# Performance work log

Hardware: AMD Instinct MI355X
Metric: run time of the kernel (lower is better)

Reference implementation:

```python
import jax, jax.numpy as jnp
import numpy as np

B, N, D, H = 4, 2048, 768, 12
DK = D // H  # 64

def setup_inputs() -> dict:
    key = jax.random.key(0)
    ks = jax.random.split(key, 7)
    f = lambda k, shape: jax.random.normal(k, shape, dtype=jnp.float32)
    return {
        "Q": f(ks[0], (B, N, D)),
        "K": f(ks[1], (B, N, D)),
        "V": f(ks[2], (B, N, D)),
        "w_q": f(ks[3], (D, D)) * 0.02,
        "w_k": f(ks[4], (D, D)) * 0.02,
        "w_v": f(ks[5], (D, D)) * 0.02,
        "w_o": f(ks[6], (D, D)) * 0.02,
    }

def reference(Q, K, V, w_q, w_k, w_v, w_o):
    # Linear with bias=False: y = x @ W.T, W is [out, in]
    def proj(x, w):
        # [B, N, D] -> [B, H, N, DK]
        y = jnp.einsum('bnd,ed->bne', x, w)
        return y.reshape(B, N, H, DK).transpose(0, 2, 1, 3)
    q = proj(Q, w_q)
    k = proj(K, w_k)
    v = proj(V, w_v)
    scale = 1.0 / jnp.sqrt(jnp.float32(DK))
    scores = jnp.einsum('bhqd,bhkd->bhqk', q, k) * scale  # [B,H,N,N]
    weights = jax.nn.softmax(scores, axis=-1)
    out = jnp.einsum('bhqk,bhkd->bhqd', weights, v)  # [B,H,N,DK]
    out = out.transpose(0, 2, 1, 3).reshape(B, N, D)
    return jnp.einsum('bnd,ed->bne', out, w_o)
```

## Files before the change

### kernel.cpp

```cpp
#include <hip/hip_runtime.h>

typedef unsigned short ushortT;
typedef __attribute__((ext_vector_type(8))) short bf16x8;
typedef __attribute__((ext_vector_type(4))) float f32x4;
typedef __attribute__((ext_vector_type(16))) float f32x16;
typedef __attribute__((ext_vector_type(2))) int i32x2;

#define QSCALE 0.18033688011112042f

__device__ __forceinline__ unsigned short f2bf(float f) {
  unsigned int u = __float_as_uint(f);
  u += 0x7FFFu + ((u >> 16) & 1u);
  return (unsigned short)(u >> 16);
}
__device__ __forceinline__ unsigned short f2bf_fast(float f) {
  unsigned int u = __float_as_uint(f) + 0x8000u;
  return (unsigned short)(u >> 16);
}

__device__ __forceinline__ void gl16(const void* g, void* l) {
  __builtin_amdgcn_global_load_lds(
      (const __attribute__((address_space(1))) void*)g,
      (__attribute__((address_space(3))) void*)l, 16, 0, 0);
}

__device__ __forceinline__ float cross_sum(float x) {
  i32x2 r = __builtin_amdgcn_permlane32_swap(__float_as_int(x), __float_as_int(x), false, false);
  return __int_as_float(r[0]) + __int_as_float(r[1]);
}
__device__ __forceinline__ unsigned cvtpk(float lo, float hi) {
  unsigned r;
  asm("v_cvt_pk_bf16_f32 %0, %1, %2" : "=v"(r) : "v"(lo), "v"(hi));
  return r;
}

__global__ __launch_bounds__(256) void cvt_all(
    const float* __restrict__ q, const float* __restrict__ k, const float* __restrict__ v,
    const float* __restrict__ w0, const float* __restrict__ w1,
    const float* __restrict__ w2, const float* __restrict__ w3,
    ushortT* xq, ushortT* xk, ushortT* xv,
    ushortT* bw0, ushortT* bw1, ushortT* bw2, ushortT* bw3) {
  int t = blockIdx.y;
  const float* src; ushortT* dst; int n;
  switch (t) {
    case 0: src = q;  dst = xq;  n = 8192 * 768; break;
    case 1: src = k;  dst = xk;  n = 8192 * 768; break;
    case 2: src = v;  dst = xv;  n = 8192 * 768; break;
    case 3: src = w0; dst = bw0; n = 768 * 768;  break;
    case 4: src = w1; dst = bw1; n = 768 * 768;  break;
    case 5: src = w2; dst = bw2; n = 768 * 768;  break;
    default: src = w3; dst = bw3; n = 768 * 768; break;
  }
  int i = (blockIdx.x * 256 + threadIdx.x) * 4;
  if (i >= n) return;
  float4 f = *(const float4*)(src + i);
  ushort4 o = make_ushort4(f2bf(f.x), f2bf(f.y), f2bf(f.z), f2bf(f.w));
  *(ushort4*)(dst + i) = o;
}

__global__ __launch_bounds__(256) void gemm_qkv(
    const ushortT* __restrict__ xq, const ushortT* __restrict__ xk,
    const ushortT* __restrict__ xv, const ushortT* __restrict__ bwq,
    const ushortT* __restrict__ bwk, const ushortT* __restrict__ bwv,
    ushortT* qp, ushortT* kp, ushortT* vtp) {
  constexpr int K = 768;
  __shared__ __attribute__((aligned(16))) ushortT As[128 * 32];
  __shared__ __attribute__((aligned(16))) ushortT Bs[128 * 32];
  const int tid = threadIdx.x;
  const int w = tid >> 6, l = tid & 63;
  const int z = blockIdx.z, bx = blockIdx.x;
  const ushortT* A;
  const ushortT* Bm;
  int m0, n0;
  if (z < 2) {
    A = z ? xk : xq; Bm = z ? bwk : bwq;
    m0 = (bx / 6) * 128; n0 = (bx % 6) * 128;
  } else {
    A = bwv; Bm = xv;
    m0 = (bx % 6) * 128; n0 = (bx / 6) * 128;
  }
  const ushortT* Ab = A  + (size_t)m0 * K;
  const ushortT* Bb = Bm + (size_t)n0 * K;

  f32x4 acc[4][4] = {};
  const int wr = w >> 1, wc = w & 1;
  const int lg = l >> 4, li = l & 15;
  const int srow = tid >> 2, scol = (tid & 3) * 8;

  for (int k0 = 0; k0 < K; k0 += 32) {
    gl16(Ab + (size_t)srow * K + (k0 + scol),        &As[w * 512]);
    gl16(Ab + (size_t)(64 + srow) * K + (k0 + scol), &As[2048 + w * 512]);
    gl16(Bb + (size_t)srow * K + (k0 + scol),        &Bs[w * 512]);
    gl16(Bb + (size_t)(64 + srow) * K + (k0 + scol), &Bs[2048 + w * 512]);
    __syncthreads();
    bf16x8 af[4], bfr[4];
#pragma unroll
    for (int mi = 0; mi < 4; ++mi)
      af[mi] = *(const bf16x8*)&As[(wr * 64 + mi * 16 + li) * 32 + lg * 8];
#pragma unroll
    for (int ni = 0; ni < 4; ++ni)
      bfr[ni] = *(const bf16x8*)&Bs[(wc * 64 + ni * 16 + li) * 32 + lg * 8];
#pragma unroll
    for (int mi = 0; mi < 4; ++mi)
#pragma unroll
      for (int ni = 0; ni < 4; ++ni)
        acc[mi][ni] = __builtin_amdgcn_mfma_f32_16x16x32_bf16(af[mi], bfr[ni], acc[mi][ni], 0, 0, 0);
    __syncthreads();
  }

  const float sc = (z == 0) ? QSCALE : 1.0f;
  ushortT* dst0 = (z == 0) ? qp : kp;
#pragma unroll
  for (int mi = 0; mi < 4; ++mi) {
#pragma unroll
    for (int ni = 0; ni < 4; ++ni) {
#pragma unroll
      for (int r = 0; r < 4; ++r) {
        int m = m0 + wr * 64 + mi * 16 + lg * 4 + r;
        int n = n0 + wc * 64 + ni * 16 + li;
        float val = acc[mi][ni][r];
        if (z < 2) {
          int b = m >> 11, nn = m & 2047, hh = n >> 6, dk = n & 63;
          dst0[(((size_t)(b * 12 + hh)) * 2048 + nn) * 64 + dk] = f2bf_fast(val * sc);
        } else {
          vtp[(size_t)m * 8192 + n] = f2bf_fast(val);
        }
      }
    }
  }
}

__global__ __launch_bounds__(256) void gemm_out(
    const ushortT* __restrict__ A0, const ushortT* __restrict__ B0, float* O0) {
  constexpr int K = 768;
  __shared__ __attribute__((aligned(16))) ushortT As[128 * 32];
  __shared__ __attribute__((aligned(16))) ushortT Bs[128 * 32];
  const int tid = threadIdx.x;
  const int w = tid >> 6, l = tid & 63;
  const int m0 = blockIdx.y * 128, n0 = blockIdx.x * 128;
  const ushortT* Ab = A0 + (size_t)m0 * K;
  const ushortT* Bb = B0 + (size_t)n0 * K;

  f32x4 acc[4][4] = {};
  const int wr = w >> 1, wc = w & 1;
  const int lg = l >> 4, li = l & 15;
  const int srow = tid >> 2, scol = (tid & 3) * 8;

  for (int k0 = 0; k0 < K; k0 += 32) {
    gl16(Ab + (size_t)srow * K + (k0 + scol),        &As[w * 512]);
    gl16(Ab + (size_t)(64 + srow) * K + (k0 + scol), &As[2048 + w * 512]);
    gl16(Bb + (size_t)srow * K + (k0 + scol),        &Bs[w * 512]);
    gl16(Bb + (size_t)(64 + srow) * K + (k0 + scol), &Bs[2048 + w * 512]);
    __syncthreads();
    bf16x8 af[4], bfr[4];
#pragma unroll
    for (int mi = 0; mi < 4; ++mi)
      af[mi] = *(const bf16x8*)&As[(wr * 64 + mi * 16 + li) * 32 + lg * 8];
#pragma unroll
    for (int ni = 0; ni < 4; ++ni)
      bfr[ni] = *(const bf16x8*)&Bs[(wc * 64 + ni * 16 + li) * 32 + lg * 8];
#pragma unroll
    for (int mi = 0; mi < 4; ++mi)
#pragma unroll
      for (int ni = 0; ni < 4; ++ni)
        acc[mi][ni] = __builtin_amdgcn_mfma_f32_16x16x32_bf16(af[mi], bfr[ni], acc[mi][ni], 0, 0, 0);
    __syncthreads();
  }

#pragma unroll
  for (int mi = 0; mi < 4; ++mi)
#pragma unroll
    for (int ni = 0; ni < 4; ++ni)
#pragma unroll
      for (int r = 0; r < 4; ++r) {
        int m = m0 + wr * 64 + mi * 16 + lg * 4 + r;
        int n = n0 + wc * 64 + ni * 16 + li;
        O0[(size_t)m * 768 + n] = acc[mi][ni][r];
      }
}

__global__ __launch_bounds__(256, 3) void attn(
    const ushortT* __restrict__ qp, const ushortT* __restrict__ kp,
    const ushortT* __restrict__ vtp, ushortT* __restrict__ ao) {
  __shared__ __attribute__((aligned(16))) ushortT Ks[128 * 64];
  __shared__ __attribute__((aligned(16))) ushortT Vs[2 * 64 * 64];
  __shared__ __attribute__((aligned(16))) ushortT Ot[4][32 * 72];
  const int tid = threadIdx.x;
  const int w = tid >> 6, l = tid & 63;
  const int lq = l & 31, h = l >> 5;

  const int flat = blockIdx.y * 16 + blockIdx.x;
  const int head = (flat & 7) * 6 + (flat >> 7);
  const int qt = (flat >> 3) & 15;
  const int bb = head / 12, hh = head % 12;
  const size_t hb = (size_t)head * 2048 * 64;
  const int q0 = qt * 128 + w * 32;

  const ushortT* kbase = kp + hb;
  const ushortT* vbase = vtp + (size_t)(hh * 64) * 8192 + (size_t)bb * 2048;

  const int srow8 = l >> 3;
  const int scol = ((l & 7) ^ srow8) << 3;

#define STAGE(kt)                                                              \
  {                                                                            \
    _Pragma("unroll") for (int j = 0; j < 4; ++j) {                            \
      int rk = (w << 5) + (j << 3) + srow8;                                    \
      gl16(kbase + (size_t)((kt) * 128 + rk) * 64 + scol,                      \
           (char*)Ks + ((w << 5) + (j << 3)) * 128);                           \
      int rv = ((w & 1) << 5) + (j << 3) + srow8;                              \
      gl16(vbase + (size_t)rv * 8192 + (kt) * 128 + (w >> 1) * 64 + scol,      \
           (char*)Vs + (w >> 1) * 8192 + (((w & 1) << 5) + (j << 3)) * 128);   \
    }                                                                          \
  }

  bf16x8 bq[4];
#pragma unroll
  for (int c = 0; c < 4; ++c)
    bq[c] = *(const bf16x8*)&qp[hb + (size_t)(q0 + lq) * 64 + c * 16 + h * 8];

  f32x16 oa0 = {}, oa1 = {};
  float lsum = 0.f;
  const int lq7 = lq & 7;

  for (int kt = 0; kt < 16; ++kt) {
    STAGE(kt);
    __syncthreads();

#pragma unroll
    for (int khalf = 0; khalf < 2; ++khalf) {
      const char* kbuf = (const char*)Ks + khalf * 8192;
      const char* vbuf = (const char*)Vs + khalf * 8192;

      f32x16 s0 = {}, s1 = {};
#pragma unroll
      for (int c = 0; c < 4; ++c) {
        bf16x8 a0 = *(const bf16x8*)(kbuf + lq * 128 + (((2 * c + h) ^ lq7) << 4));
        s0 = __builtin_amdgcn_mfma_f32_32x32x16_bf16(a0, bq[c], s0, 0, 0, 0);
      }
#pragma unroll
      for (int c = 0; c < 4; ++c) {
        bf16x8 a1 = *(const bf16x8*)(kbuf + (32 + lq) * 128 + (((2 * c + h) ^ lq7) << 4));
        s1 = __builtin_amdgcn_mfma_f32_32x32x16_bf16(a1, bq[c], s1, 0, 0, 0);
      }

#pragma unroll
      for (int r = 0; r < 16; ++r) s0[r] = exp2f(s0[r]);
#pragma unroll
      for (int r = 0; r < 16; ++r) s1[r] = exp2f(s1[r]);
      float ps = 0.f;
#pragma unroll
      for (int r = 0; r < 16; ++r) ps += s0[r] + s1[r];
      lsum += cross_sum(ps);

      unsigned c8[16];
#pragma unroll
      for (int n = 0; n < 8; ++n) c8[n]     = cvtpk(s0[2 * n], s0[2 * n + 1]);
#pragma unroll
      for (int n = 0; n < 8; ++n) c8[8 + n] = cvtpk(s1[2 * n], s1[2 * n + 1]);

#pragma unroll
      for (int kcg = 0; kcg < 4; ++kcg) {
        const unsigned* cc = &c8[(kcg >> 1) * 8 + (kcg & 1) * 4];
        i32x2 rA = __builtin_amdgcn_permlane32_swap((int)cc[0], (int)cc[2], false, false);
        i32x2 rB = __builtin_amdgcn_permlane32_swap((int)cc[1], (int)cc[3], false, false);
        union { int u4[4]; bf16x8 v8; } pb;
        pb.u4[0] = rA[0]; pb.u4[1] = rB[0]; pb.u4[2] = rA[1]; pb.u4[3] = rB[1];
        bf16x8 av0 = *(const bf16x8*)(vbuf + lq * 128 + (((2 * kcg + h) ^ lq7) << 4));
        bf16x8 av1 = *(const bf16x8*)(vbuf + (32 + lq) * 128 + (((2 * kcg + h) ^ lq7) << 4));
        oa0 = __builtin_amdgcn_mfma_f32_32x32x16_bf16(av0, pb.v8, oa0, 0, 0, 0);
        oa1 = __builtin_amdgcn_mfma_f32_32x32x16_bf16(av1, pb.v8, oa1, 0, 0, 0);
      }
    }

    __syncthreads();
  }
#undef STAGE

  ushortT* ot = Ot[w];
  float inv = 1.f / lsum;
#pragma unroll
  for (int r = 0; r < 16; ++r) {
    int d = (r & 3) + 8 * (r >> 2) + 4 * h;
    ot[lq * 72 + d]      = f2bf_fast(oa0[r] * inv);
    ot[lq * 72 + 32 + d] = f2bf_fast(oa1[r] * inv);
  }
  asm volatile("s_waitcnt lgkmcnt(0)" ::: "memory");
  __builtin_amdgcn_sched_barrier(0);
  const int tq = l >> 1, dh = (l & 1) * 32;
  const size_t orow = ((size_t)(bb * 2048 + q0 + tq)) * 768 + hh * 64 + dh;
#pragma unroll
  for (int c = 0; c < 4; ++c) {
    bf16x8 x = *(const bf16x8*)&ot[tq * 72 + dh + c * 8];
    *(bf16x8*)&ao[orow + c * 8] = x;
  }
}

extern "C" void kernel_launch(void* const* d_in, const int* in_sizes, int n_in,
                              void* d_out, int out_size, void* d_ws, size_t ws_size,
                              hipStream_t stream) {
  const float* Q  = (const float*)d_in[0];
  const float* K_ = (const float*)d_in[1];
  const float* V  = (const float*)d_in[2];
  const float* wq = (const float*)d_in[3];
  const float* wk = (const float*)d_in[4];
  const float* wv = (const float*)d_in[5];
  const float* wo = (const float*)d_in[6];

  ushortT* xq  = (ushortT*)d_ws;
  ushortT* xk  = xq  + (size_t)8192 * 768;
  ushortT* xv  = xk  + (size_t)8192 * 768;
  ushortT* bwq = xv  + (size_t)8192 * 768;
  ushortT* bwk = bwq + (size_t)768 * 768;
  ushortT* bwv = bwk + (size_t)768 * 768;
  ushortT* bwo = bwv + (size_t)768 * 768;
  ushortT* qp  = bwo + (size_t)768 * 768;
  ushortT* kp  = qp  + (size_t)8192 * 768;
  ushortT* vtp = kp  + (size_t)8192 * 768;
  ushortT* aob = vtp + (size_t)8192 * 768;

  cvt_all<<<dim3(6144, 7), 256, 0, stream>>>(Q, K_, V, wq, wk, wv, wo,
                                             xq, xk, xv, bwq, bwk, bwv, bwo);

  gemm_qkv<<<dim3(384, 1, 3), 256, 0, stream>>>(xq, xk, xv, bwq, bwk, bwv,
                                                qp, kp, vtp);

  attn<<<dim3(16, 48), 256, 0, stream>>>(qp, kp, vtp, aob);

  gemm_out<<<dim3(6, 64), 256, 0, stream>>>(aob, bwo, (float*)d_out);
}
```

Baseline: 180.6 us.

## Double GEMM K-tile depth and compute softmax row sums with an MFMA

Both projection GEMMs now stage 64-wide K slices per barrier pair instead of 32, halving the number of sync rounds and issuing more MFMAs per stage at the cost of twice the LDS per block. The attention kernel drops the per-tile VALU reduction and cross-lane swap used for the softmax denominator and instead accumulates the row sum with an extra MFMA against a vector of bf16 ones. Because that sum is taken from the bf16-rounded probabilities, it now matches the values fed to the PV product. The epilogue packs pairs of outputs with a single conversion instruction and writes 8-byte chunks to LDS.

```diff
diff --git a/kernel.cpp b/kernel.cpp
--- a/kernel.cpp
+++ b/kernel.cpp
@@ -24,10 +24,6 @@
       (__attribute__((address_space(3))) void*)l, 16, 0, 0);
 }
 
-__device__ __forceinline__ float cross_sum(float x) {
-  i32x2 r = __builtin_amdgcn_permlane32_swap(__float_as_int(x), __float_as_int(x), false, false);
-  return __int_as_float(r[0]) + __int_as_float(r[1]);
-}
 __device__ __forceinline__ unsigned cvtpk(float lo, float hi) {
   unsigned r;
   asm("v_cvt_pk_bf16_f32 %0, %1, %2" : "=v"(r) : "v"(lo), "v"(hi));
@@ -64,8 +60,8 @@
     const ushortT* __restrict__ bwk, const ushortT* __restrict__ bwv,
     ushortT* qp, ushortT* kp, ushortT* vtp) {
   constexpr int K = 768;
-  __shared__ __attribute__((aligned(16))) ushortT As[128 * 32];
-  __shared__ __attribute__((aligned(16))) ushortT Bs[128 * 32];
+  __shared__ __attribute__((aligned(16))) ushortT As[128 * 64];
+  __shared__ __attribute__((aligned(16))) ushortT Bs[128 * 64];
   const int tid = threadIdx.x;
   const int w = tid >> 6, l = tid & 63;
   const int z = blockIdx.z, bx = blockIdx.x;
@@ -85,26 +81,32 @@
   f32x4 acc[4][4] = {};
   const int wr = w >> 1, wc = w & 1;
   const int lg = l >> 4, li = l & 15;
-  const int srow = tid >> 2, scol = (tid & 3) * 8;
-
-  for (int k0 = 0; k0 < K; k0 += 32) {
-    gl16(Ab + (size_t)srow * K + (k0 + scol),        &As[w * 512]);
-    gl16(Ab + (size_t)(64 + srow) * K + (k0 + scol), &As[2048 + w * 512]);
-    gl16(Bb + (size_t)srow * K + (k0 + scol),        &Bs[w * 512]);
-    gl16(Bb + (size_t)(64 + srow) * K + (k0 + scol), &Bs[2048 + w * 512]);
-    __syncthreads();
-    bf16x8 af[4], bfr[4];
-#pragma unroll
-    for (int mi = 0; mi < 4; ++mi)
-      af[mi] = *(const bf16x8*)&As[(wr * 64 + mi * 16 + li) * 32 + lg * 8];
-#pragma unroll
-    for (int ni = 0; ni < 4; ++ni)
-      bfr[ni] = *(const bf16x8*)&Bs[(wc * 64 + ni * 16 + li) * 32 + lg * 8];
-#pragma unroll
-    for (int mi = 0; mi < 4; ++mi)
+  const int srow8 = l >> 3;
+  const int scol = (l & 7) * 8;
+
+  for (int k0 = 0; k0 < K; k0 += 64) {
+#pragma unroll
+    for (int j = 0; j < 4; ++j) {
+      int r = (w << 5) + (j << 3) + srow8;
+      gl16(Ab + (size_t)r * K + (k0 + scol), (char*)As + ((w << 5) + (j << 3)) * 128);
+      gl16(Bb + (size_t)r * K + (k0 + scol), (char*)Bs + ((w << 5) + (j << 3)) * 128);
+    }
+    __syncthreads();
+#pragma unroll
+    for (int s = 0; s < 2; ++s) {
+      bf16x8 af[4], bfr[4];
+#pragma unroll
+      for (int mi = 0; mi < 4; ++mi)
+        af[mi] = *(const bf16x8*)&As[(wr * 64 + mi * 16 + li) * 64 + s * 32 + lg * 8];
 #pragma unroll
       for (int ni = 0; ni < 4; ++ni)
-        acc[mi][ni] = __builtin_amdgcn_mfma_f32_16x16x32_bf16(af[mi], bfr[ni], acc[mi][ni], 0, 0, 0);
+        bfr[ni] = *(const bf16x8*)&Bs[(wc * 64 + ni * 16 + li) * 64 + s * 32 + lg * 8];
+#pragma unroll
+      for (int mi = 0; mi < 4; ++mi)
+#pragma unroll
+        for (int ni = 0; ni < 4; ++ni)
+          acc[mi][ni] = __builtin_amdgcn_mfma_f32_16x16x32_bf16(af[mi], bfr[ni], acc[mi][ni], 0, 0, 0);
+    }
     __syncthreads();
   }
 
@@ -133,8 +135,8 @@
 __global__ __launch_bounds__(256) void gemm_out(
     const ushortT* __restrict__ A0, const ushortT* __restrict__ B0, float* O0) {
   constexpr int K = 768;
-  __shared__ __attribute__((aligned(16))) ushortT As[128 * 32];
-  __shared__ __attribute__((aligned(16))) ushortT Bs[128 * 32];
+  __shared__ __attribute__((aligned(16))) ushortT As[128 * 64];
+  __shared__ __attribute__((aligned(16))) ushortT Bs[128 * 64];
   const int tid = threadIdx.x;
   const int w = tid >> 6, l = tid & 63;
   const int m0 = blockIdx.y * 128, n0 = blockIdx.x * 128;
@@ -144,26 +146,32 @@
   f32x4 acc[4][4] = {};
   const int wr = w >> 1, wc = w & 1;
   const int lg = l >> 4, li = l & 15;
-  const int srow = tid >> 2, scol = (tid & 3) * 8;
-
-  for (int k0 = 0; k0 < K; k0 += 32) {
-    gl16(Ab + (size_t)srow * K + (k0 + scol),        &As[w * 512]);
-    gl16(Ab + (size_t)(64 + srow) * K + (k0 + scol), &As[2048 + w * 512]);
-    gl16(Bb + (size_t)srow * K + (k0 + scol),        &Bs[w * 512]);
-    gl16(Bb + (size_t)(64 + srow) * K + (k0 + scol), &Bs[2048 + w * 512]);
-    __syncthreads();
-    bf16x8 af[4], bfr[4];
-#pragma unroll
-    for (int mi = 0; mi < 4; ++mi)
-      af[mi] = *(const bf16x8*)&As[(wr * 64 + mi * 16 + li) * 32 + lg * 8];
-#pragma unroll
-    for (int ni = 0; ni < 4; ++ni)
-      bfr[ni] = *(const bf16x8*)&Bs[(wc * 64 + ni * 16 + li) * 32 + lg * 8];
-#pragma unroll
-    for (int mi = 0; mi < 4; ++mi)
+  const int srow8 = l >> 3;
+  const int scol = (l & 7) * 8;
+
+  for (int k0 = 0; k0 < K; k0 += 64) {
+#pragma unroll
+    for (int j = 0; j < 4; ++j) {
+      int r = (w << 5) + (j << 3) + srow8;
+      gl16(Ab + (size_t)r * K + (k0 + scol), (char*)As + ((w << 5) + (j << 3)) * 128);
+      gl16(Bb + (size_t)r * K + (k0 + scol), (char*)Bs + ((w << 5) + (j << 3)) * 128);
+    }
+    __syncthreads();
+#pragma unroll
+    for (int s = 0; s < 2; ++s) {
+      bf16x8 af[4], bfr[4];
+#pragma unroll
+      for (int mi = 0; mi < 4; ++mi)
+        af[mi] = *(const bf16x8*)&As[(wr * 64 + mi * 16 + li) * 64 + s * 32 + lg * 8];
 #pragma unroll
       for (int ni = 0; ni < 4; ++ni)
-        acc[mi][ni] = __builtin_amdgcn_mfma_f32_16x16x32_bf16(af[mi], bfr[ni], acc[mi][ni], 0, 0, 0);
+        bfr[ni] = *(const bf16x8*)&Bs[(wc * 64 + ni * 16 + li) * 64 + s * 32 + lg * 8];
+#pragma unroll
+      for (int mi = 0; mi < 4; ++mi)
+#pragma unroll
+        for (int ni = 0; ni < 4; ++ni)
+          acc[mi][ni] = __builtin_amdgcn_mfma_f32_16x16x32_bf16(af[mi], bfr[ni], acc[mi][ni], 0, 0, 0);
+    }
     __syncthreads();
   }
 
@@ -219,8 +227,12 @@
   for (int c = 0; c < 4; ++c)
     bq[c] = *(const bf16x8*)&qp[hb + (size_t)(q0 + lq) * 64 + c * 16 + h * 8];
 
+  bf16x8 ones;
+#pragma unroll
+  for (int e = 0; e < 8; ++e) ones[e] = (short)0x3F80;
+
   f32x16 oa0 = {}, oa1 = {};
-  float lsum = 0.f;
+  f32x16 asum = {};
   const int lq7 = lq & 7;
 
   for (int kt = 0; kt < 16; ++kt) {
@@ -248,10 +260,6 @@
       for (int r = 0; r < 16; ++r) s0[r] = exp2f(s0[r]);
 #pragma unroll
       for (int r = 0; r < 16; ++r) s1[r] = exp2f(s1[r]);
-      float ps = 0.f;
-#pragma unroll
-      for (int r = 0; r < 16; ++r) ps += s0[r] + s1[r];
-      lsum += cross_sum(ps);
 
       unsigned c8[16];
 #pragma unroll
@@ -270,6 +278,7 @@
         bf16x8 av1 = *(const bf16x8*)(vbuf + (32 + lq) * 128 + (((2 * kcg + h) ^ lq7) << 4));
         oa0 = __builtin_amdgcn_mfma_f32_32x32x16_bf16(av0, pb.v8, oa0, 0, 0, 0);
         oa1 = __builtin_amdgcn_mfma_f32_32x32x16_bf16(av1, pb.v8, oa1, 0, 0, 0);
+        asum = __builtin_amdgcn_mfma_f32_32x32x16_bf16(ones, pb.v8, asum, 0, 0, 0);
       }
     }
 
@@ -278,12 +287,17 @@
 #undef STAGE
 
   ushortT* ot = Ot[w];
-  float inv = 1.f / lsum;
-#pragma unroll
-  for (int r = 0; r < 16; ++r) {
-    int d = (r & 3) + 8 * (r >> 2) + 4 * h;
-    ot[lq * 72 + d]      = f2bf_fast(oa0[r] * inv);
-    ot[lq * 72 + 32 + d] = f2bf_fast(oa1[r] * inv);
+  float inv = 1.f / asum[0];
+#pragma unroll
+  for (int r4 = 0; r4 < 4; ++r4) {
+    int d = 8 * r4 + 4 * h;
+    uint2 p0, p1;
+    p0.x = cvtpk(oa0[4 * r4 + 0] * inv, oa0[4 * r4 + 1] * inv);
+    p0.y = cvtpk(oa0[4 * r4 + 2] * inv, oa0[4 * r4 + 3] * inv);
+    p1.x = cvtpk(oa1[4 * r4 + 0] * inv, oa1[4 * r4 + 1] * inv);
+    p1.y = cvtpk(oa1[4 * r4 + 2] * inv, oa1[4 * r4 + 3] * inv);
+    *(uint2*)&ot[lq * 72 + d]      = p0;
+    *(uint2*)&ot[lq * 72 + 32 + d] = p1;
   }
   asm volatile("s_waitcnt lgkmcnt(0)" ::: "memory");
   __builtin_amdgcn_sched_barrier(0);
```

Result: slower. 190.3 us (+5.3%).
